# Optimization experiments

Hardware: AMD Instinct MI355X
Metric: run time of the kernel (lower is better)

The kernel has to match this reference:

```python
import jax, jax.numpy as jnp
import numpy as np
import math

B, S, D, H = 4, 2048, 1024, 16
HD = D // H  # head_size = 64


def setup_inputs() -> dict:
    key = jax.random.key(0)
    ks = jax.random.split(key, 12)
    s = 1.0 / math.sqrt(D)
    inp = {
        "query_in": jax.random.normal(ks[0], (B, S, D), jnp.float32),
        "key_in": jax.random.normal(ks[1], (B, S, D), jnp.float32),
        "values_in": jax.random.normal(ks[2], (B, S, D), jnp.float32),
        # causal mask, broadcast over batch and heads
        "mask": jnp.tril(jnp.ones((S, S), jnp.int32))[None, None],
        "Wq": jax.random.normal(ks[3], (D, D), jnp.float32) * s,
        "bq": jnp.zeros((D,), jnp.float32),
        "Wk": jax.random.normal(ks[4], (D, D), jnp.float32) * s,
        "bk": jnp.zeros((D,), jnp.float32),
        "Wv": jax.random.normal(ks[5], (D, D), jnp.float32) * s,
        "bv": jnp.zeros((D,), jnp.float32),
        "Wo": jax.random.normal(ks[6], (D, D), jnp.float32) * s,
        "bo": jnp.zeros((D,), jnp.float32),
    }
    return inp


def _heads(x):
    # [B,S,D] -> [B,H,S,HD]
    return x.reshape(B, S, H, HD).transpose(0, 2, 1, 3)


def reference(query_in, key_in, values_in, mask, Wq, bq, Wk, bk, Wv, bv, Wo, bo):
    q = _heads(query_in @ Wq.T + bq)
    k = _heads(key_in @ Wk.T + bk)
    v = _heads(values_in @ Wv.T + bv)
    # scaled dot-product scores [B,H,Sq,Sk]
    att = jnp.einsum("bhqd,bhkd->bhqk", q, k) / math.sqrt(HD)
    att = jnp.where(mask == 0, jnp.float32(-1e9), att)
    # NOTE: original module applies dropout (identity at eval / p=0) directly
    # to scores with NO softmax -- faithfully reproduced here.
    out = jnp.einsum("bhqk,bhkd->bhqd", att, v)
    out = out.transpose(0, 2, 1, 3).reshape(B, S, D)
    return out @ Wo.T + bo
```

## Files before the change

kernel.cpp:

```cpp
#include <hip/hip_runtime.h>
#include <stdint.h>

typedef unsigned short ushort_t;
typedef __bf16 bf16x8 __attribute__((ext_vector_type(8)));
typedef float f32x4 __attribute__((ext_vector_type(4)));
typedef ushort_t us4 __attribute__((ext_vector_type(4)));

#define MFMA16(a, b, c) __builtin_amdgcn_mfma_f32_16x16x32_bf16((a), (b), (c), 0, 0, 0)

constexpr int Bn = 4, Sn = 2048, Dn = 1024, Hn = 16, HDn = 64;
constexpr float SCALE = 0.125f;
constexpr float NEG = -1e9f;

__device__ __forceinline__ float bf2f(ushort_t u) {
  unsigned x = ((unsigned)u) << 16;
  return __builtin_bit_cast(float, x);
}
__device__ __forceinline__ ushort_t f2bf(float f) {
  unsigned x = __builtin_bit_cast(unsigned, f);
  x = x + 0x7FFFu + ((x >> 16) & 1u);
  return (ushort_t)(x >> 16);
}
__device__ __forceinline__ uint4 ld8_f32_bf16(const float* __restrict__ p) {
  float4 a = *(const float4*)p;
  float4 b = *(const float4*)(p + 4);
  union { ushort_t u[8]; uint4 v; } r;
  r.u[0] = f2bf(a.x); r.u[1] = f2bf(a.y); r.u[2] = f2bf(a.z); r.u[3] = f2bf(a.w);
  r.u[4] = f2bf(b.x); r.u[5] = f2bf(b.y); r.u[6] = f2bf(b.z); r.u[7] = f2bf(b.w);
  return r.v;
}
__device__ __forceinline__ void gl2lds16(const void* g, void* l) {
  __builtin_amdgcn_global_load_lds(
      (__attribute__((address_space(1))) void*)g,
      (__attribute__((address_space(3))) void*)l, 16, 0, 0);
}

__global__ __launch_bounds__(256)
void cvt_all(const float* __restrict__ xq, const float* __restrict__ xk,
             const float* __restrict__ xv, const float* __restrict__ wq,
             const float* __restrict__ wk, const float* __restrict__ wv,
             const float* __restrict__ wo, ushort_t* __restrict__ Xd,
             ushort_t* __restrict__ Wd) {
  const int bid = blockIdx.x;
  if (bid < 12288) {
    const int which = bid >> 12;
    const float* s = which == 0 ? xq : which == 1 ? xk : xv;
    size_t i = ((size_t)(bid & 4095) * 256 + threadIdx.x) * 8;
    *(uint4*)(Xd + (size_t)which * 8388608 + i) = ld8_f32_bf16(s + i);
  } else {
    const int wb = bid - 12288, which = wb >> 9;
    const float* s = which == 0 ? wq : which == 1 ? wk : which == 2 ? wv : wo;
    size_t i = ((size_t)(wb & 511) * 256 + threadIdx.x) * 8;
    *(uint4*)(Wd + (size_t)which * 1048576 + i) = ld8_f32_bf16(s + i);
  }
}

__global__ __launch_bounds__(256, 4)
void gemm_qkv(const ushort_t* __restrict__ Xb, const ushort_t* __restrict__ Wb,
              const float* __restrict__ bq, const float* __restrict__ bk,
              const float* __restrict__ bv, ushort_t* __restrict__ Qd,
              ushort_t* __restrict__ Ktd, ushort_t* __restrict__ Vtd) {
  constexpr int K = 1024;
  __shared__ __align__(16) ushort_t As[128 * 64];
  __shared__ __align__(16) ushort_t Bs[128 * 64];

  const int z = blockIdx.z;
  const ushort_t* A  = Xb + (size_t)z * 8388608;
  const ushort_t* Wt = Wb + (size_t)z * 1048576;
  const float* bias = z == 0 ? bq : z == 1 ? bk : bv;
  ushort_t* Cp = z == 0 ? Qd : z == 1 ? Ktd : Vtd;

  const int tid = threadIdx.x;
  const int lane = tid & 63, w = tid >> 6;
  const int quad = lane >> 4, l16 = lane & 15;
  const int wm = w >> 1, wn = w & 1;
  const int row0 = blockIdx.x * 128;
  const int col0 = blockIdx.y * 128;

  const int sr = lane >> 3;
  const int sg = ((lane & 7) ^ (sr & 7)) * 8;
  const ushort_t* Ab = A  + (size_t)(row0 + w * 32 + sr) * K + sg;
  const ushort_t* Bb = Wt + (size_t)(col0 + w * 32 + sr) * K + sg;

  f32x4 acc[4][4] = {};

  for (int k0 = 0; k0 < K; k0 += 64) {
    __syncthreads();
#pragma unroll
    for (int i = 0; i < 4; ++i) {
      gl2lds16(Ab + (size_t)(i * 8) * K + k0, &As[(w * 32 + i * 8) * 64]);
      gl2lds16(Bb + (size_t)(i * 8) * K + k0, &Bs[(w * 32 + i * 8) * 64]);
    }
    __syncthreads();
#pragma unroll
    for (int ks = 0; ks < 2; ++ks) {
      const int kg = ((ks * 4 + quad) ^ (l16 & 7)) * 8;
      bf16x8 af[4], bfr[4];
#pragma unroll
      for (int mt = 0; mt < 4; ++mt)
        af[mt] = *(const bf16x8*)(&As[(wm * 64 + mt * 16 + l16) * 64 + kg]);
#pragma unroll
      for (int nt = 0; nt < 4; ++nt)
        bfr[nt] = *(const bf16x8*)(&Bs[(wn * 64 + nt * 16 + l16) * 64 + kg]);
#pragma unroll
      for (int mt = 0; mt < 4; ++mt)
#pragma unroll
        for (int nt = 0; nt < 4; ++nt)
          acc[mt][nt] = MFMA16(af[mt], bfr[nt], acc[mt][nt]);
    }
  }

#pragma unroll
  for (int mt = 0; mt < 4; ++mt) {
#pragma unroll
    for (int nt = 0; nt < 4; ++nt) {
      const int col = col0 + wn * 64 + nt * 16 + l16;
      const float bv4 = bias[col];
      const int rowb = row0 + wm * 64 + mt * 16 + quad * 4;
      if (z != 0) {
        const int b = rowb >> 11, s = rowb & (Sn - 1);
        const int h = col >> 6, hd = col & 63;
        us4 pk;
#pragma unroll
        for (int r = 0; r < 4; ++r) pk[r] = f2bf(acc[mt][nt][r] + bv4);
        *(us4*)(Cp + ((size_t)((b * Hn + h) * HDn + hd)) * Sn + s) = pk;
      } else {
#pragma unroll
        for (int r = 0; r < 4; ++r) {
          const int row = rowb + r;
          const int b = row >> 11, s = row & (Sn - 1);
          const int h = col >> 6, hd = col & 63;
          Cp[(((size_t)(b * Hn + h) * Sn + s) << 6) + hd] = f2bf(acc[mt][nt][r] + bv4);
        }
      }
    }
  }
}

__global__ __launch_bounds__(256, 4)
void gemm_out(const ushort_t* __restrict__ A, const ushort_t* __restrict__ Wt,
              const float* __restrict__ bias, float* __restrict__ Cp) {
  constexpr int K = 1024;
  __shared__ __align__(16) ushort_t As[128 * 64];
  __shared__ __align__(16) ushort_t Bs[128 * 64];

  const int tid = threadIdx.x;
  const int lane = tid & 63, w = tid >> 6;
  const int quad = lane >> 4, l16 = lane & 15;
  const int wm = w >> 1, wn = w & 1;
  const int row0 = blockIdx.x * 128;
  const int col0 = blockIdx.y * 128;

  const int sr = lane >> 3;
  const int sg = ((lane & 7) ^ (sr & 7)) * 8;
  const ushort_t* Ab = A  + (size_t)(row0 + w * 32 + sr) * K + sg;
  const ushort_t* Bb = Wt + (size_t)(col0 + w * 32 + sr) * K + sg;

  f32x4 acc[4][4] = {};

  for (int k0 = 0; k0 < K; k0 += 64) {
    __syncthreads();
#pragma unroll
    for (int i = 0; i < 4; ++i) {
      gl2lds16(Ab + (size_t)(i * 8) * K + k0, &As[(w * 32 + i * 8) * 64]);
      gl2lds16(Bb + (size_t)(i * 8) * K + k0, &Bs[(w * 32 + i * 8) * 64]);
    }
    __syncthreads();
#pragma unroll
    for (int ks = 0; ks < 2; ++ks) {
      const int kg = ((ks * 4 + quad) ^ (l16 & 7)) * 8;
      bf16x8 af[4], bfr[4];
#pragma unroll
      for (int mt = 0; mt < 4; ++mt)
        af[mt] = *(const bf16x8*)(&As[(wm * 64 + mt * 16 + l16) * 64 + kg]);
#pragma unroll
      for (int nt = 0; nt < 4; ++nt)
        bfr[nt] = *(const bf16x8*)(&Bs[(wn * 64 + nt * 16 + l16) * 64 + kg]);
#pragma unroll
      for (int mt = 0; mt < 4; ++mt)
#pragma unroll
        for (int nt = 0; nt < 4; ++nt)
          acc[mt][nt] = MFMA16(af[mt], bfr[nt], acc[mt][nt]);
    }
  }

#pragma unroll
  for (int mt = 0; mt < 4; ++mt)
#pragma unroll
    for (int nt = 0; nt < 4; ++nt) {
      const int col = col0 + wn * 64 + nt * 16 + l16;
      const float bv = bias[col];
      const int rowb = row0 + wm * 64 + mt * 16 + quad * 4;
#pragma unroll
      for (int r = 0; r < 4; ++r)
        Cp[(size_t)(rowb + r) * 1024 + col] = acc[mt][nt][r] + bv;
    }
}

__global__ __launch_bounds__(256)
void gtile(const ushort_t* __restrict__ Kt, const ushort_t* __restrict__ Vt,
           float* __restrict__ Gd, float* __restrict__ Rs) {
  __shared__ __align__(16) ushort_t Kts[4096];
  __shared__ __align__(16) ushort_t Vts[4096];
  __shared__ float tsum[64];
  const int tid = threadIdx.x, lane = tid & 63, w = tid >> 6;
  const int quad = lane >> 4, l16 = lane & 15;
  const int t = blockIdx.x, bh = blockIdx.y;
  const ushort_t* Ktb = Kt + (size_t)bh * HDn * Sn;
  const ushort_t* Vtb = Vt + (size_t)bh * HDn * Sn;

  const int sr = lane >> 3;
  const int sg = ((lane & 7) ^ (sr & 7)) * 8;

  if (tid < 64) tsum[tid] = 0.f;
#pragma unroll
  for (int c = 0; c < 2; ++c) {
    const int row = w * 16 + c * 8;
    gl2lds16(Ktb + (size_t)(row + sr) * Sn + t * 64 + sg, &Kts[row * 64]);
    gl2lds16(Vtb + (size_t)(row + sr) * Sn + t * 64 + sg, &Vts[row * 64]);
  }
  __syncthreads();

  f32x4 zacc[4] = {};
#pragma unroll
  for (int ks = 0; ks < 2; ++ks) {
    const int kg = ((ks * 4 + quad) ^ (l16 & 7)) * 8;
    bf16x8 ak = *(const bf16x8*)(&Kts[(w * 16 + l16) * 64 + kg]);
#pragma unroll
    for (int nt = 0; nt < 4; ++nt) {
      bf16x8 bv8 = *(const bf16x8*)(&Vts[(nt * 16 + l16) * 64 + kg]);
      zacc[nt] = MFMA16(ak, bv8, zacc[nt]);
    }
  }
  float* gd = Gd + (size_t)(bh * 32 + t) * 4096;
#pragma unroll
  for (int nt = 0; nt < 4; ++nt)
    *(f32x4*)(gd + (nt * 16 + l16) * 64 + w * 16 + quad * 4) = zacc[nt];

  {
    const int n = tid & 63, j = tid >> 6;
    float p = 0.f;
#pragma unroll
    for (int gg2 = 0; gg2 < 2; ++gg2) {
      const int g = 2 * j + gg2;
      union { uint4 v; ushort_t u[8]; } c;
      c.v = *(const uint4*)(&Vts[n * 64 + ((g ^ (n & 7)) << 3)]);
#pragma unroll
      for (int e = 0; e < 8; ++e) p += bf2f(c.u[e]);
    }
    atomicAdd(&tsum[n], p);
  }
  __syncthreads();
  if (tid < 64) Rs[(size_t)(bh * 32 + t) * 64 + tid] = tsum[tid];
}

__global__ __launch_bounds__(256)
void scanz(const float* __restrict__ Gd, const float* __restrict__ Rs,
           ushort_t* __restrict__ Zp, float* __restrict__ suffV) {
  const int tid = threadIdx.x;
  const int nc = blockIdx.x, bh = blockIdx.y;
  const int nl = tid >> 4;
  const int n = nc * 16 + nl;
  const int d0 = (tid & 15) * 4;
  const float* gb = Gd + (size_t)bh * 32 * 4096 + n * 64 + d0;
  ushort_t* zb = Zp + (size_t)bh * 32 * 4096 + n * 64 + d0;

  f32x4 acc = {0.f, 0.f, 0.f, 0.f};
  f32x4 g0 = *(const f32x4*)(gb);
  f32x4 g1 = *(const f32x4*)(gb + 4096);
  for (int t = 0; t < 32; ++t) {
    us4 pk;
#pragma unroll
    for (int r = 0; r < 4; ++r) pk[r] = f2bf(SCALE * acc[r]);
    *(us4*)(zb + (size_t)t * 4096) = pk;
    const int tn = (t + 2 < 32) ? t + 2 : 31;
    f32x4 gn = *(const f32x4*)(gb + (size_t)tn * 4096);
    acc += g0;
    g0 = g1; g1 = gn;
  }

  __shared__ float rs[32][16];
  for (int i = tid; i < 512; i += 256)
    rs[i >> 4][i & 15] = Rs[(size_t)(bh * 32 + (i >> 4)) * 64 + nc * 16 + (i & 15)];
  __syncthreads();
  if (tid < 16) {
    float a = 0.f;
    for (int t = 31; t >= 0; --t) {
      suffV[(size_t)(bh * 32 + t) * 64 + nc * 16 + tid] = a;
      a += rs[t][tid];
    }
  }
}

__global__ __launch_bounds__(256)
void attn_kernel(const ushort_t* __restrict__ Q, const ushort_t* __restrict__ Kt,
                 const ushort_t* __restrict__ Vt, const ushort_t* __restrict__ Zp,
                 const float* __restrict__ suffV, ushort_t* __restrict__ O) {
  __shared__ __align__(16) ushort_t Vts[4096];
  __shared__ __align__(16) ushort_t Zs[4096];
  __shared__ __align__(16) ushort_t Ks[4096];
  __shared__ __align__(16) ushort_t Ss[64][72];

  const int tid = threadIdx.x, lane = tid & 63, w = tid >> 6;
  const int quad = lane >> 4, l16 = lane & 15;
  const int bh = blockIdx.x;
  const int qt = blockIdx.y, q0 = qt * 64;
  const int b = bh >> 4, h = bh & 15;
  const ushort_t* Qb  = Q  + (size_t)bh * Sn * HDn;
  const ushort_t* Ktb = Kt + (size_t)bh * HDn * Sn;
  const ushort_t* Vtb = Vt + (size_t)bh * HDn * Sn;
  const ushort_t* Zb  = Zp + (size_t)(bh * 32 + qt) * 4096;

  const int sr = lane >> 3;
  const int sg = ((lane & 7) ^ (sr & 7)) * 8;
  const int q8 = lane & 7, h8 = lane >> 3;

  uint4 kv[2];
#pragma unroll
  for (int c = 0; c < 2; ++c)
    kv[c] = *(const uint4*)(Ktb + (size_t)(w * 16 + c * 8 + h8) * Sn + q0 + q8 * 8);

#pragma unroll
  for (int c = 0; c < 2; ++c) {
    const int row = w * 16 + c * 8;
    gl2lds16(Vtb + (size_t)(row + sr) * Sn + q0 + sg, &Vts[row * 64]);
    gl2lds16(Zb + (size_t)(row + sr) * 64 + sg, &Zs[row * 64]);
  }

  bf16x8 bq[2];
#pragma unroll
  for (int ks = 0; ks < 2; ++ks)
    bq[ks] = *(const bf16x8*)(Qb + (size_t)(q0 + w * 16 + l16) * HDn + (ks * 4 + quad) * 8);

#pragma unroll
  for (int c = 0; c < 2; ++c) {
    const int hd = w * 16 + c * 8 + h8;
    const int G = hd >> 3;
    const ushort_t* ku = (const ushort_t*)&kv[c];
#pragma unroll
    for (int j = 0; j < 8; ++j) {
      const int e = (j + q8) & 7;
      const int s = q8 * 8 + e;
      Ks[s * 64 + ((G ^ e) << 3) + (hd & 7)] = ku[e];
    }
  }
  __syncthreads();

  f32x4 oacc[4] = {};
#pragma unroll
  for (int ks = 0; ks < 2; ++ks) {
    const int kg = ((ks * 4 + quad) ^ (l16 & 7)) * 8;
#pragma unroll
    for (int nt = 0; nt < 4; ++nt) {
      bf16x8 az = *(const bf16x8*)(&Zs[(nt * 16 + l16) * 64 + kg]);
      oacc[nt] = MFMA16(az, bq[ks], oacc[nt]);
    }
  }
  f32x4 sacc[4] = {};
#pragma unroll
  for (int ks = 0; ks < 2; ++ks) {
    const int kg = ((ks * 4 + quad) ^ (l16 & 7)) * 8;
#pragma unroll
    for (int nt = 0; nt < 4; ++nt) {
      bf16x8 ak = *(const bf16x8*)(&Ks[(nt * 16 + l16) * 64 + kg]);
      sacc[nt] = MFMA16(ak, bq[ks], sacc[nt]);
    }
  }
  const int qrel = w * 16 + l16;
#pragma unroll
  for (int nt = 0; nt < 4; ++nt) {
    const int kb = nt * 16 + quad * 4;
    us4 pk;
#pragma unroll
    for (int r = 0; r < 4; ++r) {
      float val = (kb + r > qrel) ? NEG : sacc[nt][r] * SCALE;
      pk[r] = f2bf(val);
    }
    *(us4*)(&Ss[qrel][kb]) = pk;
  }
#pragma unroll
  for (int ks = 0; ks < 2; ++ks) {
    bf16x8 bs = *(const bf16x8*)(&Ss[qrel][ks * 32 + quad * 8]);
#pragma unroll
    for (int nt = 0; nt < 4; ++nt) {
      bf16x8 av = *(const bf16x8*)(&Vts[(nt * 16 + l16) * 64 + (((ks * 4 + quad) ^ (l16 & 7)) << 3)]);
      oacc[nt] = MFMA16(av, bs, oacc[nt]);
    }
  }

  const float* sv = suffV + (size_t)(bh * 32 + qt) * 64;
  const int s = q0 + w * 16 + l16;
#pragma unroll
  for (int nt = 0; nt < 4; ++nt) {
    const int nb = nt * 16 + quad * 4;
    float4 s4 = *(const float4*)(sv + nb);
    us4 pk;
    pk[0] = f2bf(oacc[nt][0] + NEG * s4.x);
    pk[1] = f2bf(oacc[nt][1] + NEG * s4.y);
    pk[2] = f2bf(oacc[nt][2] + NEG * s4.z);
    pk[3] = f2bf(oacc[nt][3] + NEG * s4.w);
    *(us4*)(&O[((size_t)(b * Sn + s)) * Dn + h * 64 + nb]) = pk;
  }
}

extern "C" void kernel_launch(void* const* d_in, const int* in_sizes, int n_in,
                              void* d_out, int out_size, void* d_ws, size_t ws_size,
                              hipStream_t stream) {
  const float* Xq = (const float*)d_in[0];
  const float* Xk = (const float*)d_in[1];
  const float* Xv = (const float*)d_in[2];
  const float* Wq = (const float*)d_in[4];
  const float* bq = (const float*)d_in[5];
  const float* Wk = (const float*)d_in[6];
  const float* bk = (const float*)d_in[7];
  const float* Wv = (const float*)d_in[8];
  const float* bv = (const float*)d_in[9];
  const float* Wo = (const float*)d_in[10];
  const float* bo = (const float*)d_in[11];

  constexpr size_t MiB = 1024 * 1024;
  char* ws = (char*)d_ws;
  ushort_t* Xb  = (ushort_t*)(ws);
  ushort_t* Wb  = (ushort_t*)(ws + 48 * MiB);
  ushort_t* Qb  = (ushort_t*)(ws + 56 * MiB);
  ushort_t* Ktb = (ushort_t*)(ws + 72 * MiB);
  ushort_t* Vtb = (ushort_t*)(ws + 88 * MiB);
  ushort_t* Zp  = (ushort_t*)(ws + 104 * MiB);
  ushort_t* Ob  = (ushort_t*)(ws + 120 * MiB);
  float*    sV  = (float*)   (ws + 136 * MiB);
  float*    Gd  = (float*)   (ws + 144 * MiB);
  float*    Rsum= (float*)   (ws + 176 * MiB);

  cvt_all<<<14336, 256, 0, stream>>>(Xq, Xk, Xv, Wq, Wk, Wv, Wo, Xb, Wb);
  gemm_qkv<<<dim3(64, 8, 3), 256, 0, stream>>>(Xb, Wb, bq, bk, bv, Qb, Ktb, Vtb);
  gtile<<<dim3(32, 64), 256, 0, stream>>>(Ktb, Vtb, Gd, Rsum);
  scanz<<<dim3(4, 64), 256, 0, stream>>>(Gd, Rsum, Zp, sV);
  attn_kernel<<<dim3(64, 32), 256, 0, stream>>>(Qb, Ktb, Vtb, Zp, sV, Ob);
  gemm_out<<<dim3(64, 8), 256, 0, stream>>>(Ob, Wb + (size_t)3 * 1048576, bo,
                                            (float*)d_out);
}
```

Before: 298.1 us.

## Fuse prefix-scan of tile products into attention kernel with double-buffered tiles

Merges the scanz and attn kernels into one scan_attn kernel. Each block now handles four consecutive query tiles and rebuilds the prefix sum of G tiles directly from Gd, with the suffix sums of V computed in shared memory. This removes the Zp/suffV round trip through global memory and one launch. V, K and Q for the next tile are prefetched into double buffers. The cost is redundant prefix accumulation: later blocks re-read up to 28 G tiles, and the grid drops to 512 blocks, which lowers parallelism.

```diff
diff --git a/kernel.cpp b/kernel.cpp
--- a/kernel.cpp
+++ b/kernel.cpp
@@ -255,151 +255,173 @@
 }
 
 __global__ __launch_bounds__(256)
-void scanz(const float* __restrict__ Gd, const float* __restrict__ Rs,
-           ushort_t* __restrict__ Zp, float* __restrict__ suffV) {
-  const int tid = threadIdx.x;
-  const int nc = blockIdx.x, bh = blockIdx.y;
-  const int nl = tid >> 4;
-  const int n = nc * 16 + nl;
-  const int d0 = (tid & 15) * 4;
-  const float* gb = Gd + (size_t)bh * 32 * 4096 + n * 64 + d0;
-  ushort_t* zb = Zp + (size_t)bh * 32 * 4096 + n * 64 + d0;
-
-  f32x4 acc = {0.f, 0.f, 0.f, 0.f};
-  f32x4 g0 = *(const f32x4*)(gb);
-  f32x4 g1 = *(const f32x4*)(gb + 4096);
-  for (int t = 0; t < 32; ++t) {
-    us4 pk;
-#pragma unroll
-    for (int r = 0; r < 4; ++r) pk[r] = f2bf(SCALE * acc[r]);
-    *(us4*)(zb + (size_t)t * 4096) = pk;
-    const int tn = (t + 2 < 32) ? t + 2 : 31;
-    f32x4 gn = *(const f32x4*)(gb + (size_t)tn * 4096);
-    acc += g0;
-    g0 = g1; g1 = gn;
-  }
-
-  __shared__ float rs[32][16];
-  for (int i = tid; i < 512; i += 256)
-    rs[i >> 4][i & 15] = Rs[(size_t)(bh * 32 + (i >> 4)) * 64 + nc * 16 + (i & 15)];
-  __syncthreads();
-  if (tid < 16) {
-    float a = 0.f;
-    for (int t = 31; t >= 0; --t) {
-      suffV[(size_t)(bh * 32 + t) * 64 + nc * 16 + tid] = a;
-      a += rs[t][tid];
-    }
-  }
-}
-
-__global__ __launch_bounds__(256)
-void attn_kernel(const ushort_t* __restrict__ Q, const ushort_t* __restrict__ Kt,
-                 const ushort_t* __restrict__ Vt, const ushort_t* __restrict__ Zp,
-                 const float* __restrict__ suffV, ushort_t* __restrict__ O) {
-  __shared__ __align__(16) ushort_t Vts[4096];
+void scan_attn(const ushort_t* __restrict__ Q, const ushort_t* __restrict__ Kt,
+               const ushort_t* __restrict__ Vt, const float* __restrict__ Gd,
+               const float* __restrict__ Rs, ushort_t* __restrict__ O) {
+  __shared__ __align__(16) ushort_t Vts[2][4096];
   __shared__ __align__(16) ushort_t Zs[4096];
   __shared__ __align__(16) ushort_t Ks[4096];
   __shared__ __align__(16) ushort_t Ss[64][72];
+  __shared__ __align__(16) float sfx[4][64];
 
   const int tid = threadIdx.x, lane = tid & 63, w = tid >> 6;
   const int quad = lane >> 4, l16 = lane & 15;
   const int bh = blockIdx.x;
-  const int qt = blockIdx.y, q0 = qt * 64;
+  const int g = blockIdx.y;
+  const int qt0 = g * 4;
   const int b = bh >> 4, h = bh & 15;
   const ushort_t* Qb  = Q  + (size_t)bh * Sn * HDn;
   const ushort_t* Ktb = Kt + (size_t)bh * HDn * Sn;
   const ushort_t* Vtb = Vt + (size_t)bh * HDn * Sn;
-  const ushort_t* Zb  = Zp + (size_t)(bh * 32 + qt) * 4096;
+  const float* Gb = Gd + (size_t)bh * 32 * 4096;
+  const float* Rb = Rs + (size_t)bh * 32 * 64;
 
   const int sr = lane >> 3;
   const int sg = ((lane & 7) ^ (sr & 7)) * 8;
   const int q8 = lane & 7, h8 = lane >> 3;
 
-  uint4 kv[2];
-#pragma unroll
-  for (int c = 0; c < 2; ++c)
-    kv[c] = *(const uint4*)(Ktb + (size_t)(w * 16 + c * 8 + h8) * Sn + q0 + q8 * 8);
-
-#pragma unroll
-  for (int c = 0; c < 2; ++c) {
-    const int row = w * 16 + c * 8;
-    gl2lds16(Vtb + (size_t)(row + sr) * Sn + q0 + sg, &Vts[row * 64]);
-    gl2lds16(Zb + (size_t)(row + sr) * 64 + sg, &Zs[row * 64]);
-  }
-
-  bf16x8 bq[2];
-#pragma unroll
-  for (int ks = 0; ks < 2; ++ks)
-    bq[ks] = *(const bf16x8*)(Qb + (size_t)(q0 + w * 16 + l16) * HDn + (ks * 4 + quad) * 8);
-
-#pragma unroll
-  for (int c = 0; c < 2; ++c) {
-    const int hd = w * 16 + c * 8 + h8;
-    const int G = hd >> 3;
-    const ushort_t* ku = (const ushort_t*)&kv[c];
-#pragma unroll
-    for (int j = 0; j < 8; ++j) {
-      const int e = (j + q8) & 7;
-      const int s = q8 * 8 + e;
-      Ks[s * 64 + ((G ^ e) << 3) + (hd & 7)] = ku[e];
-    }
-  }
-  __syncthreads();
-
-  f32x4 oacc[4] = {};
-#pragma unroll
-  for (int ks = 0; ks < 2; ++ks) {
-    const int kg = ((ks * 4 + quad) ^ (l16 & 7)) * 8;
+  const int zn = tid >> 2, zd0 = (tid & 3) * 16;
+  const float* gthr = Gb + zn * 64 + zd0;
+
+  uint4  kvr[2][2];
+  bf16x8 bqr[2][2];
+  f32x4  gq[2][4];
+
+  {
+    const int q0 = qt0 * 64;
+#pragma unroll
+    for (int c = 0; c < 2; ++c) {
+      const int row = w * 16 + c * 8;
+      gl2lds16(Vtb + (size_t)(row + sr) * Sn + q0 + sg, &Vts[0][row * 64]);
+      kvr[0][c] = *(const uint4*)(Ktb + (size_t)(w * 16 + c * 8 + h8) * Sn + q0 + q8 * 8);
+    }
+#pragma unroll
+    for (int ks = 0; ks < 2; ++ks)
+      bqr[0][ks] = *(const bf16x8*)(Qb + (size_t)(q0 + w * 16 + l16) * HDn + (ks * 4 + quad) * 8);
+#pragma unroll
+    for (int j = 0; j < 4; ++j)
+      gq[0][j] = *(const f32x4*)(gthr + (size_t)qt0 * 4096 + 4 * j);
+  }
+
+  if (tid < 64) {
+    float acc = 0.f;
+    for (int tau = 31; tau >= qt0; --tau) {
+      if (tau < qt0 + 4) sfx[tau - qt0][tid] = acc;
+      acc += Rb[(size_t)tau * 64 + tid];
+    }
+  }
+
+  f32x4 Zacc[4] = {};
+#pragma unroll 4
+  for (int tau = 0; tau < qt0; ++tau) {
+#pragma unroll
+    for (int j = 0; j < 4; ++j)
+      Zacc[j] += *(const f32x4*)(gthr + (size_t)tau * 4096 + 4 * j);
+  }
+
+#pragma unroll 4
+  for (int i = 0; i < 4; ++i) {
+    const int cur = i & 1;
+    const int qt = qt0 + i, q0 = qt * 64;
+
+    __syncthreads();
+
+#pragma unroll
+    for (int j = 0; j < 4; ++j) {
+      const int d = zd0 + 4 * j;
+      us4 pk;
+#pragma unroll
+      for (int r = 0; r < 4; ++r) pk[r] = f2bf(SCALE * Zacc[j][r]);
+      *(us4*)(&Zs[zn * 64 + (((d >> 3) ^ (zn & 7)) << 3) + (d & 7)]) = pk;
+    }
+#pragma unroll
+    for (int c = 0; c < 2; ++c) {
+      const int hd = w * 16 + c * 8 + h8;
+      const int G = hd >> 3;
+      const ushort_t* ku = (const ushort_t*)&kvr[cur][c];
+#pragma unroll
+      for (int j = 0; j < 8; ++j) {
+        const int e = (j + q8) & 7;
+        const int s = q8 * 8 + e;
+        Ks[s * 64 + ((G ^ e) << 3) + (hd & 7)] = ku[e];
+      }
+    }
+
+    __syncthreads();
+
+    if (i < 3) {
+      const int q1 = (qt + 1) * 64, nxt = 1 - cur;
+#pragma unroll
+      for (int c = 0; c < 2; ++c) {
+        const int row = w * 16 + c * 8;
+        gl2lds16(Vtb + (size_t)(row + sr) * Sn + q1 + sg, &Vts[nxt][row * 64]);
+        kvr[nxt][c] = *(const uint4*)(Ktb + (size_t)(w * 16 + c * 8 + h8) * Sn + q1 + q8 * 8);
+      }
+#pragma unroll
+      for (int ks = 0; ks < 2; ++ks)
+        bqr[nxt][ks] = *(const bf16x8*)(Qb + (size_t)(q1 + w * 16 + l16) * HDn + (ks * 4 + quad) * 8);
+#pragma unroll
+      for (int j = 0; j < 4; ++j)
+        gq[nxt][j] = *(const f32x4*)(gthr + (size_t)(qt + 1) * 4096 + 4 * j);
+    }
+
+    f32x4 oacc[4] = {};
+#pragma unroll
+    for (int ks = 0; ks < 2; ++ks) {
+      const int kg = ((ks * 4 + quad) ^ (l16 & 7)) * 8;
+#pragma unroll
+      for (int nt = 0; nt < 4; ++nt) {
+        bf16x8 az = *(const bf16x8*)(&Zs[(nt * 16 + l16) * 64 + kg]);
+        oacc[nt] = MFMA16(az, bqr[cur][ks], oacc[nt]);
+      }
+    }
+    f32x4 sacc[4] = {};
+#pragma unroll
+    for (int ks = 0; ks < 2; ++ks) {
+      const int kg = ((ks * 4 + quad) ^ (l16 & 7)) * 8;
+#pragma unroll
+      for (int nt = 0; nt < 4; ++nt) {
+        bf16x8 ak = *(const bf16x8*)(&Ks[(nt * 16 + l16) * 64 + kg]);
+        sacc[nt] = MFMA16(ak, bqr[cur][ks], sacc[nt]);
+      }
+    }
+    const int qrel = w * 16 + l16;
 #pragma unroll
     for (int nt = 0; nt < 4; ++nt) {
-      bf16x8 az = *(const bf16x8*)(&Zs[(nt * 16 + l16) * 64 + kg]);
-      oacc[nt] = MFMA16(az, bq[ks], oacc[nt]);
-    }
-  }
-  f32x4 sacc[4] = {};
-#pragma unroll
-  for (int ks = 0; ks < 2; ++ks) {
-    const int kg = ((ks * 4 + quad) ^ (l16 & 7)) * 8;
+      const int kb = nt * 16 + quad * 4;
+      us4 pk;
+#pragma unroll
+      for (int r = 0; r < 4; ++r) {
+        float val = (kb + r > qrel) ? NEG : sacc[nt][r] * SCALE;
+        pk[r] = f2bf(val);
+      }
+      *(us4*)(&Ss[qrel][kb]) = pk;
+    }
+#pragma unroll
+    for (int ks = 0; ks < 2; ++ks) {
+      bf16x8 bs = *(const bf16x8*)(&Ss[qrel][ks * 32 + quad * 8]);
+#pragma unroll
+      for (int nt = 0; nt < 4; ++nt) {
+        bf16x8 av = *(const bf16x8*)(&Vts[cur][(nt * 16 + l16) * 64 + (((ks * 4 + quad) ^ (l16 & 7)) << 3)]);
+        oacc[nt] = MFMA16(av, bs, oacc[nt]);
+      }
+    }
+
+    const int s = q0 + w * 16 + l16;
 #pragma unroll
     for (int nt = 0; nt < 4; ++nt) {
-      bf16x8 ak = *(const bf16x8*)(&Ks[(nt * 16 + l16) * 64 + kg]);
-      sacc[nt] = MFMA16(ak, bq[ks], sacc[nt]);
-    }
-  }
-  const int qrel = w * 16 + l16;
-#pragma unroll
-  for (int nt = 0; nt < 4; ++nt) {
-    const int kb = nt * 16 + quad * 4;
-    us4 pk;
-#pragma unroll
-    for (int r = 0; r < 4; ++r) {
-      float val = (kb + r > qrel) ? NEG : sacc[nt][r] * SCALE;
-      pk[r] = f2bf(val);
-    }
-    *(us4*)(&Ss[qrel][kb]) = pk;
-  }
-#pragma unroll
-  for (int ks = 0; ks < 2; ++ks) {
-    bf16x8 bs = *(const bf16x8*)(&Ss[qrel][ks * 32 + quad * 8]);
-#pragma unroll
-    for (int nt = 0; nt < 4; ++nt) {
-      bf16x8 av = *(const bf16x8*)(&Vts[(nt * 16 + l16) * 64 + (((ks * 4 + quad) ^ (l16 & 7)) << 3)]);
-      oacc[nt] = MFMA16(av, bs, oacc[nt]);
-    }
-  }
-
-  const float* sv = suffV + (size_t)(bh * 32 + qt) * 64;
-  const int s = q0 + w * 16 + l16;
-#pragma unroll
-  for (int nt = 0; nt < 4; ++nt) {
-    const int nb = nt * 16 + quad * 4;
-    float4 s4 = *(const float4*)(sv + nb);
-    us4 pk;
-    pk[0] = f2bf(oacc[nt][0] + NEG * s4.x);
-    pk[1] = f2bf(oacc[nt][1] + NEG * s4.y);
-    pk[2] = f2bf(oacc[nt][2] + NEG * s4.z);
-    pk[3] = f2bf(oacc[nt][3] + NEG * s4.w);
-    *(us4*)(&O[((size_t)(b * Sn + s)) * Dn + h * 64 + nb]) = pk;
+      const int nb = nt * 16 + quad * 4;
+      float4 s4 = *(const float4*)(&sfx[i][nb]);
+      us4 pk;
+      pk[0] = f2bf(oacc[nt][0] + NEG * s4.x);
+      pk[1] = f2bf(oacc[nt][1] + NEG * s4.y);
+      pk[2] = f2bf(oacc[nt][2] + NEG * s4.z);
+      pk[3] = f2bf(oacc[nt][3] + NEG * s4.w);
+      *(us4*)(&O[((size_t)(b * Sn + s)) * Dn + h * 64 + nb]) = pk;
+    }
+
+#pragma unroll
+    for (int j = 0; j < 4; ++j) Zacc[j] += gq[cur][j];
   }
 }
 
@@ -425,17 +447,14 @@
   ushort_t* Qb  = (ushort_t*)(ws + 56 * MiB);
   ushort_t* Ktb = (ushort_t*)(ws + 72 * MiB);
   ushort_t* Vtb = (ushort_t*)(ws + 88 * MiB);
-  ushort_t* Zp  = (ushort_t*)(ws + 104 * MiB);
   ushort_t* Ob  = (ushort_t*)(ws + 120 * MiB);
-  float*    sV  = (float*)   (ws + 136 * MiB);
   float*    Gd  = (float*)   (ws + 144 * MiB);
   float*    Rsum= (float*)   (ws + 176 * MiB);
 
   cvt_all<<<14336, 256, 0, stream>>>(Xq, Xk, Xv, Wq, Wk, Wv, Wo, Xb, Wb);
   gemm_qkv<<<dim3(64, 8, 3), 256, 0, stream>>>(Xb, Wb, bq, bk, bv, Qb, Ktb, Vtb);
   gtile<<<dim3(32, 64), 256, 0, stream>>>(Ktb, Vtb, Gd, Rsum);
-  scanz<<<dim3(4, 64), 256, 0, stream>>>(Gd, Rsum, Zp, sV);
-  attn_kernel<<<dim3(64, 32), 256, 0, stream>>>(Qb, Ktb, Vtb, Zp, sV, Ob);
+  scan_attn<<<dim3(64, 8), 256, 0, stream>>>(Qb, Ktb, Vtb, Gd, Rsum, Ob);
   gemm_out<<<dim3(64, 8), 256, 0, stream>>>(Ob, Wb + (size_t)3 * 1048576, bo,
                                             (float*)d_out);
 }
```

Measured after the change: 303.5 us. No clear change (+1.8%).
